# Kernel tuning notes

Measured on AMD Instinct MI355X. Metric: run time of the kernel, lower is better.

The kernel has to match this reference:

```python
import jax, jax.numpy as jnp
import numpy as np

B_SZ, SEQ = 2, 4096
D_MODEL = 1024
EXPAND = 2
HEADDIM = 64
D_STATE = 128
D_CONV = 4
INTER = EXPAND * D_MODEL            # 2048
NHEADS = INTER // HEADDIM           # 32
CONV_DIM = INTER + 2 * D_STATE      # n_groups = 1
PROJ_DIM = 2 * INTER + 2 * D_STATE + NHEADS
CHUNK = 256
EPS = 1e-5


def setup_inputs() -> dict:
    key = jax.random.key(0)
    k = jax.random.split(key, 6)
    u = jax.random.normal(k[0], (B_SZ, SEQ, D_MODEL), jnp.float32)
    in_proj_w = jax.random.normal(k[1], (D_MODEL, PROJ_DIM), jnp.float32) * 0.02
    conv_w = jax.random.normal(k[2], (CONV_DIM, D_CONV), jnp.float32) * 0.2
    conv_b = jnp.zeros((CONV_DIM,), jnp.float32)
    # dt init in [1e-3, 1e-1], inverse-softplus so softplus(dt_bias) recovers dt
    dt0 = jnp.exp(jax.random.uniform(k[3], (NHEADS,), jnp.float32, np.log(1e-3), np.log(1e-1)))
    dt_bias = jnp.log(jnp.expm1(dt0))
    A_log = jnp.log(jnp.arange(1, NHEADS + 1, dtype=jnp.float32))
    D_param = jnp.ones((NHEADS,), jnp.float32)
    norm_w = jnp.ones((INTER,), jnp.float32)
    out_proj_w = jax.random.normal(k[4], (INTER, D_MODEL), jnp.float32) * 0.02
    return {"u": u, "in_proj_w": in_proj_w, "conv_w": conv_w, "conv_b": conv_b,
            "dt_bias": dt_bias, "A_log": A_log, "D_param": D_param,
            "norm_w": norm_w, "out_proj_w": out_proj_w}


def _silu(x):
    return x * jax.nn.sigmoid(x)


def _causal_conv1d(x, w, b):
    # depthwise causal conv; x (b,s,c), w (c,k); tap k-1 is the current timestep
    k = w.shape[1]
    xp = jnp.pad(x, ((0, 0), (k - 1, 0), (0, 0)))
    y = b
    for i in range(k):
        y = y + xp[:, i:i + x.shape[1], :] * w[:, i]
    return y


def _segsum(x):
    # x (..., l) -> (..., l, l); segsum[i, j] = sum_{j < k <= i} x[k], -inf above diag
    l = x.shape[-1]
    cs = jnp.cumsum(x, -1)
    d = cs[..., :, None] - cs[..., None, :]
    mask = jnp.tril(jnp.ones((l, l), dtype=bool))
    return jnp.where(mask, d, -jnp.inf)


def _ssd(x, dt, A, Bm, Cm):
    # Mamba-2 chunked SSD (ssd_minimal_discrete with X = x*dt, Adt = A*dt).
    # x (b,s,h,p), dt (b,s,h), A (h,), Bm/Cm (b,s,n)
    b, s, h, p = x.shape
    n = Bm.shape[-1]
    c = s // CHUNK
    X = (x * dt[..., None]).reshape(b, c, CHUNK, h, p)          # (b,c,l,h,p)
    Adt = (dt * A).reshape(b, c, CHUNK, h).transpose(0, 3, 1, 2)  # (b,h,c,l)
    Bc = Bm.reshape(b, c, CHUNK, n)
    Cc = Cm.reshape(b, c, CHUNK, n)
    A_cum = jnp.cumsum(Adt, -1)                                  # (b,h,c,l)
    L = jnp.exp(_segsum(Adt))                                    # (b,h,c,l,l) causal decay
    # intra-chunk (diagonal blocks)
    scores = jnp.einsum('bcln,bcsn->bcls', Cc, Bc)               # (b,c,l,l)
    Y_diag = jnp.einsum('bhcls,bcshp->bclhp', scores[:, None] * L, X)
    # per-chunk final states
    decay_states = jnp.exp(A_cum[..., -1:] - A_cum)              # (b,h,c,l)
    states = jnp.einsum('bcln,bhcl,bclhp->bchpn', Bc, decay_states, X)
    # inter-chunk recurrence on chunk states
    A_chunk = jnp.pad(A_cum[..., -1], ((0, 0), (0, 0), (1, 0)))  # (b,h,c+1)
    decay_chunk = jnp.exp(_segsum(A_chunk))                      # (b,h,c+1,c+1)
    states = jnp.concatenate([jnp.zeros_like(states[:, :1]), states], axis=1)  # (b,c+1,h,p,n)
    states = jnp.einsum('bhzc,bchpn->bzhpn', decay_chunk, states)[:, :-1]      # (b,c,h,p,n)
    # state -> output contribution
    Y_off = jnp.einsum('bcln,bchpn,bhcl->bclhp', Cc, states, jnp.exp(A_cum))
    return (Y_diag + Y_off).reshape(b, s, h, p)


def reference(u, in_proj_w, conv_w, conv_b, dt_bias, A_log, D_param, norm_w, out_proj_w):
    b, s, _ = u.shape
    zxbcdt = u @ in_proj_w                                       # (b,s,PROJ_DIM)
    z = zxbcdt[..., :INTER]
    xBC = zxbcdt[..., INTER:INTER + CONV_DIM]
    dt = zxbcdt[..., INTER + CONV_DIM:]
    xBC = _silu(_causal_conv1d(xBC, conv_w, conv_b))
    x = xBC[..., :INTER]
    Bm = xBC[..., INTER:INTER + D_STATE]
    Cm = xBC[..., INTER + D_STATE:]
    dt = jax.nn.softplus(dt + dt_bias)                           # (b,s,h)
    A = -jnp.exp(A_log)                                          # (h,)
    xh = x.reshape(b, s, NHEADS, HEADDIM)
    y = _ssd(xh, dt, A, Bm, Cm) + D_param[None, None, :, None] * xh
    y = y.reshape(b, s, INTER)
    g = y * _silu(z)                                             # gated RMSNorm
    g = g * jax.lax.rsqrt(jnp.mean(g * g, -1, keepdims=True) + EPS) * norm_w
    return g @ out_proj_w
```

## Files before the change

kernel.cpp:

```cpp
#include <hip/hip_runtime.h>
#include <hip/hip_bf16.h>

#define B_SZ 2
#define SEQ 4096
#define DMODEL 1024
#define INTER 2048
#define NHEADS 32
#define HDIM 64
#define DSTATE 128
#define DCONV 4
#define CONVDIM 2304
#define PROJDIM 4384
#define CHUNK 256
#define NCHUNK 16
#define ROWS (B_SZ*SEQ)
#define NGEMM 4352
#define NMAIN 4096

typedef __hip_bfloat16 bf16;
typedef short bfx8 __attribute__((ext_vector_type(8)));
typedef float f32x4 __attribute__((ext_vector_type(4)));

__device__ __forceinline__ float sigmoidf_(float x){ return 1.f/(1.f+expf(-x)); }
__device__ __forceinline__ float b2f(bf16 v){ return __bfloat162float(v); }
__device__ __forceinline__ bf16 f2b(float v){ return __float2bfloat16(v); }
__device__ __forceinline__ float bits2f(unsigned short u){ return __uint_as_float(((unsigned)u) << 16); }
__device__ __forceinline__ unsigned short f2bits(float v){ bf16 t = __float2bfloat16(v); return *(unsigned short*)&t; }

#define MFMA16(a,b,c) __builtin_amdgcn_mfma_f32_16x16x32_bf16(a,b,c,0,0,0)

__global__ void zero_out_kernel(float* o, int n){
  int i = blockIdx.x*256 + threadIdx.x;
  if (i < n) o[i] = 0.f;
}

__global__ __launch_bounds__(256) void transcast2_kernel(const float* __restrict__ w_in,
    bf16* __restrict__ w_inT, const float* __restrict__ w_out, bf16* __restrict__ w_outT){
  __shared__ float t[64][65];
  int blk = blockIdx.x, tid = threadIdx.x;
  const float* in; bf16* outT; int R, ld, c0, r0;
  if (blk < 1088){
    in = w_in;  outT = w_inT;  R = DMODEL; ld = PROJDIM;
    c0 = (blk % 68)*64; r0 = (blk / 68)*64;
  } else {
    int i = blk - 1088;
    in = w_out; outT = w_outT; R = INTER;  ld = DMODEL;
    c0 = (i & 15)*64;   r0 = (i >> 4)*64;
  }
  #pragma unroll
  for (int i = 0; i < 16; i++){
    int idx = tid + i*256;
    int r = idx >> 6, c = idx & 63;
    t[r][c] = in[(size_t)(r0+r)*ld + c0 + c];
  }
  __syncthreads();
  #pragma unroll
  for (int i = 0; i < 16; i++){
    int idx = tid + i*256;
    int c = idx >> 6, r = idx & 63;
    outT[(size_t)(c0+c)*R + r0 + r] = f2b(t[r][c]);
  }
}

__device__ __forceinline__ void stage8(const bf16* __restrict__ g, int Kdim,
    int tile0, int k0, char* region, int h, int tid){
  #pragma unroll
  for (int l = 0; l < 2; l++){
    int o  = h*16384 + (l*512 + tid)*16;
    int os = o ^ (((o >> 7) & 7) << 4);
    const bf16* src = g + (size_t)(tile0 + (os >> 7))*Kdim + k0 + ((os & 127) >> 1);
    __builtin_amdgcn_global_load_lds(
      (const __attribute__((address_space(1))) void*)src,
      (__attribute__((address_space(3))) void*)(region + h*16384 + (l*512 + (tid >> 6)*64)*16),
      16, 0, 0);
  }
}
__device__ __forceinline__ bfx8 fr8(const char* region, int row, int colbyte){
  int o = row*128 + colbyte;
  o ^= ((row & 7) << 4);
  return *(const bfx8*)(region + o);
}

#define LGKM0  asm volatile("s_waitcnt lgkmcnt(0)" ::: "memory"); __builtin_amdgcn_sched_barrier(0)
#define VM4    asm volatile("s_waitcnt vmcnt(4)" ::: "memory")
#define VM0    asm volatile("s_waitcnt vmcnt(0)" ::: "memory")
#define BAR    __builtin_amdgcn_s_barrier()
#define PRIO1  __builtin_amdgcn_s_setprio(1)
#define PRIO0  __builtin_amdgcn_s_setprio(0)

#define MFMA_QUAD(MH, NH, BARR)                                                \
  PRIO1;                                                                       \
  _Pragma("unroll") for (int m = 0; m < 4; m++)                                \
    _Pragma("unroll") for (int n = 0; n < 2; n++)                              \
      _Pragma("unroll") for (int kk = 0; kk < 2; kk++)                         \
        acc[(MH)+m][(NH)+n] = MFMA16(aF[m][kk], BARR[n][kk], acc[(MH)+m][(NH)+n]); \
  PRIO0

#define GEMM8_BODY(K_, NBX_)                                                   \
  extern __shared__ char lds[];                                                \
  char* A0 = lds;          char* B0 = lds + 32768;                             \
  char* A1 = lds + 65536;  char* B1 = lds + 98304;                             \
  const int tid = threadIdx.x, lane = tid & 63, wid = tid >> 6;                \
  const int wm = wid >> 2, wn = wid & 3;                                       \
  int nb = (blockIdx.x & 7)*((int)gridDim.x >> 3) + (blockIdx.x >> 3);         \
  const int bx = nb % (NBX_), by = nb / (NBX_);                                \
  const int row0 = by*256, col0 = bx*256;                                      \
  f32x4 acc[8][4] = {};                                                        \
  bfx8 aF[4][2], b01[2][2], b23[2][2];                                         \
  const int frow = lane & 15;                                                  \
  const int fcb0 = (lane >> 4)*16;                                             \
  const int JLAST = (K_)/128 - 1;                                              \
  stage8(Bt, K_, col0, 0,  B0, 0, tid);                                        \
  stage8(Bt, K_, col0, 0,  B0, 1, tid);                                        \
  stage8(A,  K_, row0, 0,  A0, 0, tid);                                        \
  stage8(A,  K_, row0, 0,  A0, 1, tid);                                        \
  stage8(Bt, K_, col0, 64, B1, 0, tid);                                        \
  stage8(Bt, K_, col0, 64, B1, 1, tid);                                        \
  VM4;                                                                         \
  BAR;                                                                         \
  _Pragma("unroll 1")                                                          \
  for (int j = 0; j <= JLAST; j++){                                            \
    const int kO  = j*128 + 64;                                                \
    const int kS1 = (j*128 + 128) & ((K_) - 1);                                \
    const int kS2 = (j*128 + 192) & ((K_) - 1);                                \
    stage8(A, K_, row0, kO, A1, 0, tid);                                       \
    _Pragma("unroll") for (int m = 0; m < 4; m++)                              \
      _Pragma("unroll") for (int kk = 0; kk < 2; kk++)                         \
        aF[m][kk] = fr8(A0, wm*128 + m*16 + frow, kk*64 + fcb0);               \
    _Pragma("unroll") for (int n = 0; n < 2; n++)                              \
      _Pragma("unroll") for (int kk = 0; kk < 2; kk++)                         \
        b01[n][kk] = fr8(B0, wn*64 + n*16 + frow, kk*64 + fcb0);               \
    LGKM0;                                                                     \
    MFMA_QUAD(0, 0, b01);                                                      \
    BAR;                                                                       \
    stage8(A, K_, row0, kO, A1, 1, tid);                                       \
    _Pragma("unroll") for (int n = 0; n < 2; n++)                              \
      _Pragma("unroll") for (int kk = 0; kk < 2; kk++)                         \
        b23[n][kk] = fr8(B0, wn*64 + (n+2)*16 + frow, kk*64 + fcb0);           \
    LGKM0;                                                                     \
    MFMA_QUAD(0, 2, b23);                                                      \
    BAR;                                                                       \
    if (j < JLAST) stage8(Bt, K_, col0, kS1, B0, 0, tid);                      \
    _Pragma("unroll") for (int m = 0; m < 4; m++)                              \
      _Pragma("unroll") for (int kk = 0; kk < 2; kk++)                         \
        aF[m][kk] = fr8(A0, wm*128 + (m+4)*16 + frow, kk*64 + fcb0);           \
    LGKM0;                                                                     \
    MFMA_QUAD(4, 0, b01);                                                      \
    BAR;                                                                       \
    if (j < JLAST){ stage8(Bt, K_, col0, kS1, B0, 1, tid); VM4; }              \
    else { VM0; }                                                              \
    MFMA_QUAD(4, 2, b23);                                                      \
    BAR;                                                                       \
    if (j < JLAST) stage8(A, K_, row0, kS1, A0, 0, tid);                       \
    _Pragma("unroll") for (int m = 0; m < 4; m++)                              \
      _Pragma("unroll") for (int kk = 0; kk < 2; kk++)                         \
        aF[m][kk] = fr8(A1, wm*128 + m*16 + frow, kk*64 + fcb0);               \
    _Pragma("unroll") for (int n = 0; n < 2; n++)                              \
      _Pragma("unroll") for (int kk = 0; kk < 2; kk++)                         \
        b01[n][kk] = fr8(B1, wn*64 + n*16 + frow, kk*64 + fcb0);               \
    LGKM0;                                                                     \
    MFMA_QUAD(0, 0, b01);                                                      \
    BAR;                                                                       \
    if (j < JLAST) stage8(A, K_, row0, kS1, A0, 1, tid);                       \
    _Pragma("unroll") for (int n = 0; n < 2; n++)                              \
      _Pragma("unroll") for (int kk = 0; kk < 2; kk++)                         \
        b23[n][kk] = fr8(B1, wn*64 + (n+2)*16 + frow, kk*64 + fcb0);           \
    LGKM0;                                                                     \
    MFMA_QUAD(0, 2, b23);                                                      \
    BAR;                                                                       \
    if (j < JLAST) stage8(Bt, K_, col0, kS2, B1, 0, tid);                      \
    _Pragma("unroll") for (int m = 0; m < 4; m++)                              \
      _Pragma("unroll") for (int kk = 0; kk < 2; kk++)                         \
        aF[m][kk] = fr8(A1, wm*128 + (m+4)*16 + frow, kk*64 + fcb0);           \
    LGKM0;                                                                     \
    MFMA_QUAD(4, 0, b01);                                                      \
    BAR;                                                                       \
    if (j < JLAST) stage8(Bt, K_, col0, kS2, B1, 1, tid);                      \
    VM4;                                                                       \
    MFMA_QUAD(4, 2, b23);                                                      \
    BAR;                                                                       \
  }

#define SST_STRIDE 280

__global__ __launch_bounds__(512, 2) void gemm8_inproj(const bf16* __restrict__ A,
    const bf16* __restrict__ Bt, bf16* __restrict__ z, bf16* __restrict__ xbc){
  GEMM8_BODY(DMODEL, 16)
  unsigned short* sst = (unsigned short*)lds;
  #pragma unroll 1
  for (int half = 0; half < 2; half++){
    if (wm == half){
      #pragma unroll
      for (int m = 0; m < 8; m++)
        #pragma unroll
        for (int n = 0; n < 4; n++)
          #pragma unroll
          for (int r = 0; r < 4; r++){
            int rl = m*16 + (lane>>4)*4 + r;
            sst[rl*SST_STRIDE + wn*64 + n*16 + (lane&15)] = f2bits(acc[m][n][r]);
          }
    }
    BAR;
    #pragma unroll
    for (int i = 0; i < 8; i++){
      int q = tid + i*512;
      int rl = q >> 5, c8 = (q & 31)*8;
      bfx8 v = *(const bfx8*)(sst + rl*SST_STRIDE + c8);
      int gr = row0 + half*128 + rl, gc = col0 + c8;
      if (gc < INTER) *(bfx8*)(z + (size_t)gr*INTER + gc) = v;
      else            *(bfx8*)(xbc + (size_t)gr*CONVDIM + (gc - INTER)) = v;
    }
    BAR;
  }
}

#define MFMA_GEMM_BODY(K_, ROW0_, COL0_, EPILOGUE)                             \
  __shared__ unsigned short As[128*64];                                        \
  __shared__ unsigned short Bs[128*64];                                        \
  const int tid = threadIdx.x;                                                 \
  const int lane = tid & 63, wid = tid >> 6;                                   \
  const int wm = wid >> 1, wn = wid & 1;                                       \
  const int row0 = (ROW0_), col0 = (COL0_);                                    \
  f32x4 acc[4][4] = {};                                                        \
  const int rstg = wid*32 + ((lane>>3)&7);                                     \
  const int kstg = (lane&7)*8;                                                 \
  for (int k0 = 0; k0 < (K_); k0 += 64){                                       \
    _Pragma("unroll")                                                          \
    for (int j = 0; j < 4; j++){                                               \
      const bf16* gA = A + (size_t)(row0 + rstg + j*8)*(K_) + k0 + kstg;       \
      __builtin_amdgcn_global_load_lds(                                        \
        (const __attribute__((address_space(1))) void*)gA,                     \
        (__attribute__((address_space(3))) void*)(As + (wid*32 + j*8)*64),     \
        16, 0, 0);                                                             \
      const bf16* gB = Bt + (size_t)(col0 + rstg + j*8)*(K_) + k0 + kstg;      \
      __builtin_amdgcn_global_load_lds(                                        \
        (const __attribute__((address_space(1))) void*)gB,                     \
        (__attribute__((address_space(3))) void*)(Bs + (wid*32 + j*8)*64),     \
        16, 0, 0);                                                             \
    }                                                                          \
    __syncthreads();                                                           \
    _Pragma("unroll")                                                          \
    for (int kk = 0; kk < 2; kk++){                                            \
      bfx8 af[4], bfr[4];                                                      \
      _Pragma("unroll")                                                        \
      for (int m = 0; m < 4; m++)                                              \
        af[m] = *(const bfx8*)(As + (wm*64 + m*16 + (lane&15))*64              \
                               + kk*32 + (lane>>4)*8);                         \
      _Pragma("unroll")                                                        \
      for (int n = 0; n < 4; n++)                                              \
        bfr[n] = *(const bfx8*)(Bs + (wn*64 + n*16 + (lane&15))*64             \
                                + kk*32 + (lane>>4)*8);                        \
      _Pragma("unroll")                                                        \
      for (int m = 0; m < 4; m++)                                              \
        _Pragma("unroll")                                                      \
        for (int n = 0; n < 4; n++)                                            \
          acc[m][n] = MFMA16(af[m], bfr[n], acc[m][n]);                        \
    }                                                                          \
    __syncthreads();                                                           \
  }                                                                            \
  _Pragma("unroll")                                                            \
  for (int m = 0; m < 4; m++){                                                 \
    int row = row0 + wm*64 + m*16 + (lane>>4)*4;                               \
    _Pragma("unroll")                                                          \
    for (int n = 0; n < 4; n++){                                               \
      int col = col0 + wn*64 + n*16 + (lane&15);                               \
      _Pragma("unroll")                                                        \
      for (int r = 0; r < 4; r++){                                             \
        float v = acc[m][n][r];                                                \
        int rr = row + r;                                                      \
        EPILOGUE                                                               \
      }                                                                        \
    }                                                                          \
  }

__global__ __launch_bounds__(256) void gemm_mfma_inproj(const bf16* __restrict__ A,
    const bf16* __restrict__ Bt, bf16* __restrict__ z, bf16* __restrict__ xbc){
  MFMA_GEMM_BODY(DMODEL, blockIdx.y*128, blockIdx.x*128,
    if (col < INTER) z[(size_t)rr*INTER + col] = f2b(v);
    else             xbc[(size_t)rr*CONVDIM + (col - INTER)] = f2b(v);
  )
}
__global__ __launch_bounds__(256) void gemm_mfma_strip(const bf16* __restrict__ A,
    const bf16* __restrict__ Bt, bf16* __restrict__ xbc){
  MFMA_GEMM_BODY(DMODEL, blockIdx.y*128, blockIdx.x*128,
    xbc[(size_t)rr*CONVDIM + 2048 + col] = f2b(v);
  )
}
__global__ __launch_bounds__(256) void gemm_mfma_outproj(const bf16* __restrict__ A,
    const bf16* __restrict__ Bt, float* __restrict__ C){
  int nbo = (blockIdx.x & 7)*64 + (blockIdx.x >> 3);
  MFMA_GEMM_BODY(INTER, (nbo >> 3)*128, (nbo & 7)*128,
    C[(size_t)rr*DMODEL + col] = v;
  )
}

__global__ __launch_bounds__(256) void dt_partial(const float* __restrict__ u,
    const float* __restrict__ w_in, float* __restrict__ partial,
    unsigned short* __restrict__ u_bf){
  __shared__ float wsm[128][33];
  __shared__ float us[32][133];
  int ks = blockIdx.x, row0 = blockIdx.y*32;
  int k0 = ks*128;
  int tid = threadIdx.x;
  #pragma unroll
  for (int i = 0; i < 16; i++){
    int idx = tid + i*256;
    wsm[idx >> 5][idx & 31] = w_in[(size_t)(k0 + (idx >> 5))*PROJDIM + NGEMM + (idx & 31)];
  }
  #pragma unroll
  for (int i = 0; i < 4; i++){
    int idx = tid + i*256;
    int r = idx >> 5, c4 = idx & 31;
    float4 v = *(const float4*)(u + (size_t)(row0 + r)*DMODEL + k0 + c4*4);
    us[r][c4*4+0] = v.x; us[r][c4*4+1] = v.y; us[r][c4*4+2] = v.z; us[r][c4*4+3] = v.w;
    ushort4 w;
    w.x = f2bits(v.x); w.y = f2bits(v.y); w.z = f2bits(v.z); w.w = f2bits(v.w);
    *(ushort4*)(u_bf + (size_t)(row0 + r)*DMODEL + k0 + c4*4) = w;
  }
  __syncthreads();
  int col = tid & 31, r0 = tid >> 5;
  float acc[4] = {};
  #pragma unroll 4
  for (int kk4 = 0; kk4 < 32; kk4++){
    float4 uv[4];
    #pragma unroll
    for (int i = 0; i < 4; i++)
      uv[i] = *(const float4*)&us[r0 + i*8][kk4*4];
    #pragma unroll
    for (int j = 0; j < 4; j++){
      float wv = wsm[kk4*4 + j][col];
      #pragma unroll
      for (int i = 0; i < 4; i++){
        float uvj = (j == 0) ? uv[i].x : (j == 1) ? uv[i].y : (j == 2) ? uv[i].z : uv[i].w;
        acc[i] = fmaf(uvj, wv, acc[i]);
      }
    }
  }
  #pragma unroll
  for (int i = 0; i < 4; i++)
    partial[((size_t)ks*ROWS + row0 + r0 + i*8)*NHEADS + col] = acc[i];
}

__global__ __launch_bounds__(256) void conv_kernel(const bf16* __restrict__ xbc,
    const float* __restrict__ cw, const float* __restrict__ cb,
    bf16* __restrict__ x, bf16* __restrict__ Bm, bf16* __restrict__ Cm){
  int ch = blockIdx.x*256 + threadIdx.x;
  int t0 = blockIdx.y*64;
  int b  = blockIdx.z;
  float w0 = cw[ch*4+0], w1 = cw[ch*4+1], w2 = cw[ch*4+2], w3 = cw[ch*4+3];
  float bia = cb[ch];
  const bf16* src = xbc + (size_t)(b*SEQ)*CONVDIM + ch;
  float xm3 = 0.f, xm2 = 0.f, xm1 = 0.f;
  if (t0 > 0){
    xm3 = b2f(src[(size_t)(t0-3)*CONVDIM]);
    xm2 = b2f(src[(size_t)(t0-2)*CONVDIM]);
    xm1 = b2f(src[(size_t)(t0-1)*CONVDIM]);
  }
  bf16* dst; size_t dstride;
  if (ch < INTER)             { dst = x  + (size_t)(b*SEQ + t0)*INTER  + ch;                 dstride = INTER; }
  else if (ch < INTER+DSTATE) { dst = Bm + (size_t)(b*SEQ + t0)*DSTATE + (ch-INTER);         dstride = DSTATE; }
  else                        { dst = Cm + (size_t)(b*SEQ + t0)*DSTATE + (ch-INTER-DSTATE);  dstride = DSTATE; }
  #pragma unroll 4
  for (int i = 0; i < 64; i++){
    float xc = b2f(src[(size_t)(t0+i)*CONVDIM]);
    float acc = bia;
    acc = fmaf(xm3, w0, acc);
    acc = fmaf(xm2, w1, acc);
    acc = fmaf(xm1, w2, acc);
    acc = fmaf(xc,  w3, acc);
    float v = acc * sigmoidf_(acc);
    dst[(size_t)i*dstride] = f2b(v);
    xm3 = xm2; xm2 = xm1; xm1 = xc;
  }
}

__global__ __launch_bounds__(256) void acum_fused(const float* __restrict__ partial,
    const float* __restrict__ dt_bias, const float* __restrict__ A_log,
    float* __restrict__ dt, float* __restrict__ Acum){
  int bi = blockIdx.x;
  int c = bi & 15; int h = (bi >> 4) & 31; int b = bi >> 9;
  int l = threadIdx.x;
  __shared__ float sbuf[CHUNK];
  int t = c*CHUNK + l;
  size_t idx = (size_t)(b*SEQ + t)*NHEADS + h;
  float s = dt_bias[h];
  #pragma unroll
  for (int ks = 0; ks < 8; ks++)
    s += partial[(size_t)ks*ROWS*NHEADS + idx];
  float v = (s > 20.f) ? s : log1pf(expf(s));
  dt[idx] = v;
  float A = -expf(A_log[h]);
  sbuf[l] = v * A;
  __syncthreads();
  for (int off = 1; off < CHUNK; off <<= 1){
    float add = (l >= off) ? sbuf[l-off] : 0.f;
    __syncthreads();
    sbuf[l] += add;
    __syncthreads();
  }
  Acum[(size_t)bi*CHUNK + l] = sbuf[l];
}

__global__ __launch_bounds__(256) void scores_mfma(const bf16* __restrict__ Bm,
    const bf16* __restrict__ Cm, bf16* __restrict__ S){
  int bc = blockIdx.x;
  int b = bc >> 4, c = bc & 15;
  int tid = threadIdx.x, lane = tid & 63;
  int task = blockIdx.y*4 + (tid >> 6);
  if (task >= 10) return;
  int rb = (task >= 6) ? 3 : (task >= 3) ? 2 : (task >= 1) ? 1 : 0;
  int j = task - rb*(rb+1)/2;
  const bf16* Crow = Cm + (size_t)(b*SEQ + c*CHUNK)*DSTATE;
  const bf16* Brow = Bm + (size_t)(b*SEQ + c*CHUNK)*DSTATE;
  f32x4 acc[4][4] = {};
  #pragma unroll
  for (int kk = 0; kk < 4; kk++){
    bfx8 af[4], bfr[4];
    #pragma unroll
    for (int m = 0; m < 4; m++)
      af[m] = *(const bfx8*)(Crow + (size_t)(rb*64 + m*16 + (lane&15))*DSTATE + kk*32 + (lane>>4)*8);
    #pragma unroll
    for (int n = 0; n < 4; n++)
      bfr[n] = *(const bfx8*)(Brow + (size_t)(j*64 + n*16 + (lane&15))*DSTATE + kk*32 + (lane>>4)*8);
    #pragma unroll
    for (int m = 0; m < 4; m++)
      #pragma unroll
      for (int n = 0; n < 4; n++)
        acc[m][n] = MFMA16(af[m], bfr[n], acc[m][n]);
  }
  bf16* dst = S + (size_t)bc*CHUNK*CHUNK;
  #pragma unroll
  for (int m = 0; m < 4; m++)
    #pragma unroll
    for (int n = 0; n < 4; n++)
      #pragma unroll
      for (int r = 0; r < 4; r++)
        dst[(size_t)(rb*64 + m*16 + (lane>>4)*4 + r)*CHUNK + j*64 + n*16 + (lane&15)]
          = f2b(acc[m][n][r]);
}

__global__ __launch_bounds__(256) void xwt_kernel(const bf16* __restrict__ x,
    const bf16* __restrict__ Bm, const float* __restrict__ dt,
    const float* __restrict__ Acum, bf16* __restrict__ xwt, bf16* __restrict__ bt){
  int pt = blockIdx.x, tt = blockIdx.y, b = blockIdx.z;
  int tid = threadIdx.x;
  __shared__ unsigned short tile[64][72];
  __shared__ float wf[64];
  int t0 = tt*64;
  if (pt < 32){
    int h = pt, c = t0 >> 8;
    if (tid < 64){
      const float* AcB = Acum + ((size_t)(b*NHEADS + h)*NCHUNK + c)*CHUNK;
      int t = t0 + tid;
      wf[tid] = dt[(size_t)(b*SEQ + t)*NHEADS + h] * expf(AcB[255] - AcB[t & 255]);
    }
    __syncthreads();
    const bf16* src = x + (size_t)(b*SEQ + t0)*INTER + pt*64;
    #pragma unroll
    for (int i = 0; i < 2; i++){
      int u = tid + i*256;
      int r = u >> 3, po = (u & 7)*8;
      bfx8 v = *(const bfx8*)(src + (size_t)r*INTER + po);
      float d = wf[r];
      #pragma unroll
      for (int j = 0; j < 8; j++)
        tile[r][po + j] = f2bits(bits2f((unsigned short)v[j]) * d);
    }
    __syncthreads();
    bf16* dst = xwt + ((size_t)(b*INTER) + pt*64)*SEQ + t0;
    #pragma unroll
    for (int i = 0; i < 2; i++){
      int u = tid + i*256;
      int p = u >> 3, tc = (u & 7)*8;
      bfx8 v;
      #pragma unroll
      for (int j = 0; j < 8; j++) v[j] = (short)tile[tc + j][p];
      *(bfx8*)(dst + (size_t)p*SEQ + tc) = v;
    }
  } else {
    int n0 = (pt - 32)*64;
    const bf16* src = Bm + (size_t)(b*SEQ + t0)*DSTATE + n0;
    #pragma unroll
    for (int i = 0; i < 2; i++){
      int u = tid + i*256;
      int r = u >> 3, po = (u & 7)*8;
      bfx8 v = *(const bfx8*)(src + (size_t)r*DSTATE + po);
      *(bfx8*)&tile[r][po] = v;
    }
    __syncthreads();
    bf16* dst = bt + ((size_t)(b*DSTATE) + n0)*SEQ + t0;
    #pragma unroll
    for (int i = 0; i < 2; i++){
      int u = tid + i*256;
      int p = u >> 3, tc = (u & 7)*8;
      bfx8 v;
      #pragma unroll
      for (int j = 0; j < 8; j++) v[j] = (short)tile[tc + j][p];
      *(bfx8*)(dst + (size_t)p*SEQ + tc) = v;
    }
  }
}

__global__ __launch_bounds__(256) void chunk_states_mfma(const bf16* __restrict__ xwt,
    const bf16* __restrict__ bt, float* __restrict__ states){
  int bi = blockIdx.x;
  int h = bi & 31; int c = (bi >> 5) & 15; int b = bi >> 9;
  int tid = threadIdx.x, lane = tid & 63, w = tid >> 6;
  int wm = w >> 1, wn = w & 1;
  const bf16* Arow = xwt + ((size_t)(b*INTER) + h*64)*SEQ + c*CHUNK;
  const bf16* Brow = bt + (size_t)(b*DSTATE)*SEQ + c*CHUNK;
  f32x4 acc[2][4] = {};
  #pragma unroll
  for (int kk = 0; kk < 8; kk++){
    bfx8 af[2], bfr[4];
    #pragma unroll
    for (int m = 0; m < 2; m++)
      af[m] = *(const bfx8*)(Arow + (size_t)(wm*32 + m*16 + (lane&15))*SEQ + kk*32 + (lane>>4)*8);
    #pragma unroll
    for (int n = 0; n < 4; n++)
      bfr[n] = *(const bfx8*)(Brow + (size_t)(wn*64 + n*16 + (lane&15))*SEQ + kk*32 + (lane>>4)*8);
    #pragma unroll
    for (int m = 0; m < 2; m++)
      #pragma unroll
      for (int n = 0; n < 4; n++)
        acc[m][n] = MFMA16(af[m], bfr[n], acc[m][n]);
  }
  float* dst = states + (size_t)bi*HDIM*DSTATE;
  #pragma unroll
  for (int m = 0; m < 2; m++)
    #pragma unroll
    for (int n = 0; n < 4; n++)
      #pragma unroll
      for (int r = 0; r < 4; r++){
        int p = wm*32 + m*16 + (lane>>4)*4 + r;
        int nn = wn*64 + n*16 + (lane&15);
        dst[(size_t)p*DSTATE + nn] = acc[m][n][r];
      }
}

__global__ __launch_bounds__(256) void scan_kernel(float* __restrict__ states,
    const float* __restrict__ Acum){
  int idx = blockIdx.x*256 + threadIdx.x;
  int n = idx & 127; int p = (idx >> 7) & 63; int h = (idx >> 13) & 31; int b = idx >> 18;
  float R = 0.f;
  for (int c = 0; c < NCHUNK; c++){
    size_t o = (((size_t)((b*NCHUNK + c)*NHEADS + h))*HDIM + p)*DSTATE + n;
    float s = states[o];
    states[o] = R;
    float dA = expf(Acum[((size_t)(b*NHEADS + h)*NCHUNK + c)*CHUNK + CHUNK-1]);
    R = R*dA + s;
  }
}

__global__ __launch_bounds__(256, 3) void ydiag_mfma(
    const bf16* x, const float* __restrict__ dt,
    const float* __restrict__ Acum, const bf16* __restrict__ Sg,
    const bf16* __restrict__ Cm, const float* __restrict__ states,
    const float* __restrict__ Dp, bf16* y){
  int bi = blockIdx.x;
  int h = bi & 31; int c = (bi >> 5) & 15; int b = bi >> 9;
  int bc = b*NCHUNK + c;
  int tid = threadIdx.x, lane = tid & 63, w = tid >> 6;

  __shared__ unsigned short XdtT[64*264];
  __shared__ unsigned short pool[128*72];
  __shared__ float Acs[CHUNK];
  __shared__ float dts[CHUNK];

  const float* AcBase = Acum + ((size_t)(b*NHEADS + h)*NCHUNK + c)*CHUNK;
  Acs[tid] = AcBase[tid];
  dts[tid] = dt[(size_t)(b*SEQ + c*CHUNK + tid)*NHEADS + h];
  {
    const float* src = states + (size_t)bi*HDIM*DSTATE;
    #pragma unroll
    for (int i = 0; i < 8; i++){
      int q = tid + i*256;
      float4 v = ((const float4*)src)[q];
      int p = q >> 5, n = (q & 31)*4;
      ushort4 o;
      o.x = f2bits(v.x); o.y = f2bits(v.y); o.z = f2bits(v.z); o.w = f2bits(v.w);
      *(ushort4*)(pool + p*136 + n) = o;
    }
  }
  __syncthreads();

  const bf16* Crow = Cm + (size_t)(b*SEQ + c*CHUNK)*DSTATE;

  f32x4 accY[4][4] = {};
  #pragma unroll
  for (int kk = 0; kk < 4; kk++){
    bfx8 af[4], bfr[4];
    #pragma unroll
    for (int m = 0; m < 4; m++)
      af[m] = *(const bfx8*)(Crow + (size_t)(w*64 + m*16 + (lane&15))*DSTATE + kk*32 + (lane>>4)*8);
    #pragma unroll
    for (int n = 0; n < 4; n++)
      bfr[n] = *(const bfx8*)(pool + (n*16 + (lane&15))*136 + kk*32 + (lane>>4)*8);
    #pragma unroll
    for (int m = 0; m < 4; m++)
      #pragma unroll
      for (int n = 0; n < 4; n++)
        accY[m][n] = MFMA16(af[m], bfr[n], accY[m][n]);
  }
  {
    float eAl[4][4];
    #pragma unroll
    for (int m = 0; m < 4; m++)
      #pragma unroll
      for (int r = 0; r < 4; r++)
        eAl[m][r] = expf(Acs[w*64 + m*16 + (lane>>4)*4 + r]);
    #pragma unroll
    for (int m = 0; m < 4; m++)
      #pragma unroll
      for (int n = 0; n < 4; n++)
        #pragma unroll
        for (int r = 0; r < 4; r++)
          accY[m][n][r] *= eAl[m][r];
  }
  __syncthreads();

  #pragma unroll 1
  for (int q = 0; q < 2; q++){
    const bf16* xg = x + (size_t)(b*SEQ + c*CHUNK + q*128)*INTER + h*HDIM;
    #pragma unroll
    for (int i = 0; i < 4; i++){
      int u = tid + i*256;
      int s = u >> 3, p0 = (u & 7)*8;
      bfx8 v = *(const bfx8*)(xg + (size_t)s*INTER + p0);
      float d = dts[q*128 + s];
      bfx8 o;
      #pragma unroll
      for (int j = 0; j < 8; j++)
        o[j] = (short)f2bits(bits2f((unsigned short)v[j]) * d);
      *(bfx8*)(pool + s*72 + p0) = o;
    }
    __syncthreads();
    {
      int p = tid & 63, sb = tid >> 6;
      #pragma unroll
      for (int i = 0; i < 4; i++){
        int s0 = (sb + i*4)*8;
        bfx8 v;
        #pragma unroll
        for (int j = 0; j < 8; j++)
          v[j] = (short)pool[(s0 + j)*72 + p];
        *(bfx8*)(XdtT + p*264 + q*128 + s0) = v;
      }
    }
    __syncthreads();
  }

  const bf16* Srow = Sg + (size_t)bc*CHUNK*CHUNK + (size_t)(w*64)*CHUNK;
  float Dh = Dp[h];
  for (int j = 0; j <= w; j++){
    int s0 = j*64;
    bfx8 wfr[4][2];
    if (j < w){
      float m_ = Acs[s0 + 63];
      float rowf[4];
      #pragma unroll
      for (int m = 0; m < 4; m++)
        rowf[m] = expf(Acs[w*64 + m*16 + (lane&15)] - m_);
      #pragma unroll
      for (int kk = 0; kk < 2; kk++){
        float colf[8];
        #pragma unroll
        for (int t = 0; t < 8; t++)
          colf[t] = expf(m_ - Acs[s0 + kk*32 + (lane>>4)*8 + t]);
        #pragma unroll
        for (int m = 0; m < 4; m++){
          bfx8 raw = *(const bfx8*)(Srow + (size_t)(m*16 + (lane&15))*CHUNK + s0 + kk*32 + (lane>>4)*8);
          bfx8 o;
          #pragma unroll
          for (int t = 0; t < 8; t++)
            o[t] = (short)f2bits(bits2f((unsigned short)raw[t]) * rowf[m] * colf[t]);
          wfr[m][kk] = o;
        }
      }
    } else {
      #pragma unroll
      for (int kk = 0; kk < 2; kk++)
        #pragma unroll
        for (int m = 0; m < 4; m++){
          int lg = w*64 + m*16 + (lane&15);
          float Al = Acs[lg];
          bfx8 raw = *(const bfx8*)(Srow + (size_t)(m*16 + (lane&15))*CHUNK + s0 + kk*32 + (lane>>4)*8);
          bfx8 o;
          #pragma unroll
          for (int t = 0; t < 8; t++){
            int sg = s0 + kk*32 + (lane>>4)*8 + t;
            float v;
            if (sg > lg)       v = 0.f;
            else if (sg == lg) v = bits2f((unsigned short)raw[t]) + Dh/dts[lg];
            else               v = bits2f((unsigned short)raw[t]) * expf(Al - Acs[sg]);
            o[t] = (short)f2bits(v);
          }
          wfr[m][kk] = o;
        }
    }
    #pragma unroll
    for (int kk = 0; kk < 2; kk++){
      bfx8 bfr[4];
      #pragma unroll
      for (int n = 0; n < 4; n++)
        bfr[n] = *(const bfx8*)(XdtT + (n*16 + (lane&15))*264 + s0 + kk*32 + (lane>>4)*8);
      #pragma unroll
      for (int m = 0; m < 4; m++)
        #pragma unroll
        for (int n = 0; n < 4; n++)
          accY[m][n] = MFMA16(wfr[m][kk], bfr[n], accY[m][n]);
    }
  }
  bf16* yg = y + (size_t)(b*SEQ + c*CHUNK)*INTER + h*HDIM;
  #pragma unroll
  for (int m = 0; m < 4; m++)
    #pragma unroll
    for (int n = 0; n < 4; n++)
      #pragma unroll
      for (int r = 0; r < 4; r++)
        yg[(size_t)(w*64 + m*16 + (lane>>4)*4 + r)*INTER + n*16 + (lane&15)]
          = f2b(accY[m][n][r]);
}

__global__ __launch_bounds__(256) void gatenorm_kernel(bf16* __restrict__ y,
    const bf16* __restrict__ z, const float* __restrict__ nw){
  int row = blockIdx.x;
  const bf16* zr = z + (size_t)row*INTER;
  bf16* yr = y + (size_t)row*INTER;
  int tid = threadIdx.x;
  bfx8 zv = *(const bfx8*)(zr + tid*8);
  bfx8 yv = *(const bfx8*)(yr + tid*8);
  float g[8]; float ss = 0.f;
  #pragma unroll
  for (int j = 0; j < 8; j++){
    float zf = bits2f((unsigned short)zv[j]);
    float gv = bits2f((unsigned short)yv[j]) * zf * sigmoidf_(zf);
    g[j] = gv; ss += gv*gv;
  }
  #pragma unroll
  for (int off = 32; off > 0; off >>= 1) ss += __shfl_down(ss, off);
  __shared__ float red[4];
  __shared__ float stot;
  int lane = tid & 63, wid = tid >> 6;
  if (lane == 0) red[wid] = ss;
  __syncthreads();
  if (tid == 0) stot = rsqrtf((red[0]+red[1]+red[2]+red[3]) * (1.f/INTER) + 1e-5f);
  __syncthreads();
  float sc = stot;
  float4 nw0 = *(const float4*)(nw + tid*8);
  float4 nw1 = *(const float4*)(nw + tid*8 + 4);
  bfx8 o;
  o[0] = (short)f2bits(g[0]*sc*nw0.x);
  o[1] = (short)f2bits(g[1]*sc*nw0.y);
  o[2] = (short)f2bits(g[2]*sc*nw0.z);
  o[3] = (short)f2bits(g[3]*sc*nw0.w);
  o[4] = (short)f2bits(g[4]*sc*nw1.x);
  o[5] = (short)f2bits(g[5]*sc*nw1.y);
  o[6] = (short)f2bits(g[6]*sc*nw1.z);
  o[7] = (short)f2bits(g[7]*sc*nw1.w);
  *(bfx8*)(yr + tid*8) = o;
}

extern "C" void kernel_launch(void* const* d_in, const int* in_sizes, int n_in,
                              void* d_out, int out_size, void* d_ws, size_t ws_size,
                              hipStream_t stream){
  const float* u    = (const float*)d_in[0];
  const float* w_in = (const float*)d_in[1];
  const float* cw   = (const float*)d_in[2];
  const float* cb   = (const float*)d_in[3];
  const float* dtb  = (const float*)d_in[4];
  const float* Alog = (const float*)d_in[5];
  const float* Dp   = (const float*)d_in[6];
  const float* nw   = (const float*)d_in[7];
  const float* w_out= (const float*)d_in[8];
  float* out = (float*)d_out;
  char* ws = (char*)d_ws;

  const size_t OFF_Z     = 0;
  const size_t OFF_XBC   = 33554432;
  const size_t OFF_DT    = 67108864;
  const size_t OFF_ACUM  = 68157440;
  const size_t OFF_X     = 71303168;
  const size_t OFF_UBF   = 104857600;
  const size_t OFF_WINT  = 121634816;
  const size_t OFF_XWT   = 104857600;
  const size_t OFF_BM    = 138412032;
  const size_t OFF_CM    = 140509184;
  const size_t OFF_BT    = 143654912;
  const size_t OFF_WOUTT = 145752064;
  const size_t OFF_PART  = 149946368;
  const size_t NEED      = 158334976;

  if (ws_size < NEED){
    zero_out_kernel<<<(out_size + 255)/256, 256, 0, stream>>>(out, out_size);
    return;
  }

  bf16*  z      = (bf16*)(ws + OFF_Z);
  bf16*  xbc    = (bf16*)(ws + OFF_XBC);
  float* states = (float*)(ws + OFF_XBC);
  float* dt     = (float*)(ws + OFF_DT);
  float* Acum   = (float*)(ws + OFF_ACUM);
  bf16*  x      = (bf16*)(ws + OFF_X);
  bf16*  y      = (bf16*)(ws + OFF_X);
  bf16*  u_bf   = (bf16*)(ws + OFF_UBF);
  bf16*  w_inT  = (bf16*)(ws + OFF_WINT);
  bf16*  xwt    = (bf16*)(ws + OFF_XWT);
  bf16*  Bm     = (bf16*)(ws + OFF_BM);
  bf16*  Cm     = (bf16*)(ws + OFF_CM);
  bf16*  bt     = (bf16*)(ws + OFF_BT);
  bf16*  w_outT = (bf16*)(ws + OFF_WOUTT);
  float* part   = (float*)(ws + OFF_PART);
  bf16*  S      = (bf16*)(ws + OFF_PART);

  bool use8 = true;
  if (hipFuncSetAttribute((const void*)gemm8_inproj,
        hipFuncAttributeMaxDynamicSharedMemorySize, 131072) != hipSuccess) use8 = false;

  dt_partial<<<dim3(8, ROWS/32), 256, 0, stream>>>(u, w_in, part, (unsigned short*)u_bf);
  transcast2_kernel<<<1600, 256, 0, stream>>>(w_in, w_inT, w_out, w_outT);
  if (use8){
    gemm8_inproj<<<512, 512, 131072, stream>>>(u_bf, w_inT, z, xbc);
    gemm_mfma_strip<<<dim3(2, ROWS/128), 256, 0, stream>>>(u_bf, w_inT + (size_t)NMAIN*DMODEL, xbc);
  } else {
    gemm_mfma_inproj<<<dim3(NGEMM/128, ROWS/128), 256, 0, stream>>>(u_bf, w_inT, z, xbc);
  }
  conv_kernel<<<dim3(9, SEQ/64, B_SZ), 256, 0, stream>>>(xbc, cw, cb, x, Bm, Cm);
  acum_fused<<<B_SZ*NHEADS*NCHUNK, 256, 0, stream>>>(part, dtb, Alog, dt, Acum);
  scores_mfma<<<dim3(B_SZ*NCHUNK, 3), 256, 0, stream>>>(Bm, Cm, S);
  xwt_kernel<<<dim3(34, 64, 2), 256, 0, stream>>>(x, Bm, dt, Acum, xwt, bt);
  chunk_states_mfma<<<B_SZ*NCHUNK*NHEADS, 256, 0, stream>>>(xwt, bt, states);
  scan_kernel<<<(B_SZ*NHEADS*HDIM*DSTATE)/256, 256, 0, stream>>>(states, Acum);
  ydiag_mfma<<<B_SZ*NCHUNK*NHEADS, 256, 0, stream>>>(x, dt, Acum, S, Cm, states, Dp, y);
  gatenorm_kernel<<<ROWS, 256, 0, stream>>>(y, z, nw);
  gemm_mfma_outproj<<<512, 256, 0, stream>>>(y, w_outT, out);
}
```

Measured before the change: 343.0 us.

## Interleave chunk rows across warps to balance causal diagonal work

Row ownership in the chunk-output kernel changes from contiguous 64-row slabs per warp to interleaved 16-row slices (row = m*64 + w*16). Each warp now does similar work across the lower-triangular intra-chunk matmul, where before the last warp did four times the MFMA work of the first. The X fragments are loaded once per column block and shared across row tiles. The cost is a compile-time-unrolled loop with a runtime skip that may raise register pressure, and scattered row stores.

```diff
diff --git a/kernel.cpp b/kernel.cpp
--- a/kernel.cpp
+++ b/kernel.cpp
@@ -592,7 +592,7 @@
     bfx8 af[4], bfr[4];
     #pragma unroll
     for (int m = 0; m < 4; m++)
-      af[m] = *(const bfx8*)(Crow + (size_t)(w*64 + m*16 + (lane&15))*DSTATE + kk*32 + (lane>>4)*8);
+      af[m] = *(const bfx8*)(Crow + (size_t)(m*64 + w*16 + (lane&15))*DSTATE + kk*32 + (lane>>4)*8);
     #pragma unroll
     for (int n = 0; n < 4; n++)
       bfr[n] = *(const bfx8*)(pool + (n*16 + (lane&15))*136 + kk*32 + (lane>>4)*8);
@@ -608,7 +608,7 @@
     for (int m = 0; m < 4; m++)
       #pragma unroll
       for (int r = 0; r < 4; r++)
-        eAl[m][r] = expf(Acs[w*64 + m*16 + (lane>>4)*4 + r]);
+        eAl[m][r] = expf(Acs[m*64 + w*16 + (lane>>4)*4 + r]);
     #pragma unroll
     for (int m = 0; m < 4; m++)
       #pragma unroll
@@ -650,65 +650,63 @@
     __syncthreads();
   }
 
-  const bf16* Srow = Sg + (size_t)bc*CHUNK*CHUNK + (size_t)(w*64)*CHUNK;
+  const bf16* Sbase = Sg + (size_t)bc*CHUNK*CHUNK;
   float Dh = Dp[h];
-  for (int j = 0; j <= w; j++){
+  #pragma unroll 1
+  for (int j = 0; j < 4; j++){
     int s0 = j*64;
-    bfx8 wfr[4][2];
-    if (j < w){
-      float m_ = Acs[s0 + 63];
-      float rowf[4];
-      #pragma unroll
-      for (int m = 0; m < 4; m++)
-        rowf[m] = expf(Acs[w*64 + m*16 + (lane&15)] - m_);
-      #pragma unroll
-      for (int kk = 0; kk < 2; kk++){
-        float colf[8];
+    bfx8 bfr[4][2];
+    #pragma unroll
+    for (int kk = 0; kk < 2; kk++)
+      #pragma unroll
+      for (int n = 0; n < 4; n++)
+        bfr[n][kk] = *(const bfx8*)(XdtT + (n*16 + (lane&15))*264 + s0 + kk*32 + (lane>>4)*8);
+    float m_ = Acs[s0 + 63];
+    float colf[2][8];
+    #pragma unroll
+    for (int kk = 0; kk < 2; kk++)
+      #pragma unroll
+      for (int t = 0; t < 8; t++)
+        colf[kk][t] = expf(m_ - Acs[s0 + kk*32 + (lane>>4)*8 + t]);
+    #pragma unroll
+    for (int m = 3; m >= 0; m--){
+      if (m < j) continue;
+      int lrow = m*64 + w*16 + (lane&15);
+      bfx8 wfr[2];
+      if (j < m){
+        float rowf = expf(Acs[lrow] - m_);
         #pragma unroll
-        for (int t = 0; t < 8; t++)
-          colf[t] = expf(m_ - Acs[s0 + kk*32 + (lane>>4)*8 + t]);
-        #pragma unroll
-        for (int m = 0; m < 4; m++){
-          bfx8 raw = *(const bfx8*)(Srow + (size_t)(m*16 + (lane&15))*CHUNK + s0 + kk*32 + (lane>>4)*8);
+        for (int kk = 0; kk < 2; kk++){
+          bfx8 raw = *(const bfx8*)(Sbase + (size_t)lrow*CHUNK + s0 + kk*32 + (lane>>4)*8);
           bfx8 o;
           #pragma unroll
           for (int t = 0; t < 8; t++)
-            o[t] = (short)f2bits(bits2f((unsigned short)raw[t]) * rowf[m] * colf[t]);
-          wfr[m][kk] = o;
+            o[t] = (short)f2bits(bits2f((unsigned short)raw[t]) * rowf * colf[kk][t]);
+          wfr[kk] = o;
         }
-      }
-    } else {
-      #pragma unroll
-      for (int kk = 0; kk < 2; kk++)
+      } else {
+        float Al = Acs[lrow];
         #pragma unroll
-        for (int m = 0; m < 4; m++){
-          int lg = w*64 + m*16 + (lane&15);
-          float Al = Acs[lg];
-          bfx8 raw = *(const bfx8*)(Srow + (size_t)(m*16 + (lane&15))*CHUNK + s0 + kk*32 + (lane>>4)*8);
+        for (int kk = 0; kk < 2; kk++){
+          bfx8 raw = *(const bfx8*)(Sbase + (size_t)lrow*CHUNK + s0 + kk*32 + (lane>>4)*8);
           bfx8 o;
           #pragma unroll
           for (int t = 0; t < 8; t++){
             int sg = s0 + kk*32 + (lane>>4)*8 + t;
             float v;
-            if (sg > lg)       v = 0.f;
-            else if (sg == lg) v = bits2f((unsigned short)raw[t]) + Dh/dts[lg];
-            else               v = bits2f((unsigned short)raw[t]) * expf(Al - Acs[sg]);
+            if (sg > lrow)       v = 0.f;
+            else if (sg == lrow) v = bits2f((unsigned short)raw[t]) + Dh/dts[lrow];
+            else                 v = bits2f((unsigned short)raw[t]) * expf(Al - Acs[sg]);
             o[t] = (short)f2bits(v);
           }
-          wfr[m][kk] = o;
+          wfr[kk] = o;
         }
-    }
-    #pragma unroll
-    for (int kk = 0; kk < 2; kk++){
-      bfx8 bfr[4];
-      #pragma unroll
-      for (int n = 0; n < 4; n++)
-        bfr[n] = *(const bfx8*)(XdtT + (n*16 + (lane&15))*264 + s0 + kk*32 + (lane>>4)*8);
-      #pragma unroll
-      for (int m = 0; m < 4; m++)
+      }
+      #pragma unroll
+      for (int kk = 0; kk < 2; kk++)
         #pragma unroll
         for (int n = 0; n < 4; n++)
-          accY[m][n] = MFMA16(wfr[m][kk], bfr[n], accY[m][n]);
+          accY[m][n] = MFMA16(wfr[kk], bfr[n][kk], accY[m][n]);
     }
   }
   bf16* yg = y + (size_t)(b*SEQ + c*CHUNK)*INTER + h*HDIM;
@@ -718,7 +716,7 @@
     for (int n = 0; n < 4; n++)
       #pragma unroll
       for (int r = 0; r < 4; r++)
-        yg[(size_t)(w*64 + m*16 + (lane>>4)*4 + r)*INTER + n*16 + (lane&15)]
+        yg[(size_t)(m*64 + w*16 + (lane>>4)*4 + r)*INTER + n*16 + (lane&15)]
           = f2b(accY[m][n][r]);
 }
 
```

New measurement: 349.2 us. About the same (+1.8%).
